# Performance work log

Measured on AMD Instinct MI355X. Metric: run time of the kernel, lower is better.

## Reference

```python
import jax, jax.numpy as jnp
import numpy as np

B, S, E = 32, 128, 128
NQ, NS = 100000, 512
QN, SN = 4, 10
S_MAX = 4
NEG = -1e30


def setup_inputs() -> dict:
    key = jax.random.key(0)
    ks = jax.random.split(key, 24)
    def nrm(k, shape, sc):
        return jax.random.normal(k, shape, jnp.float32) * sc
    inp = {}
    inp['question'] = jax.random.randint(ks[0], (B, S), 0, NQ, jnp.int32)
    inp['response'] = jax.random.randint(ks[1], (B, S), 0, 2, jnp.int32)
    inp['mask'] = jax.random.randint(ks[2], (B, S), 0, 2, jnp.int32)
    inp['q_neighbors'] = jax.random.randint(ks[3], (NQ, QN), 0, NS, jnp.int32)
    inp['s_neighbors'] = jax.random.randint(ks[4], (NS, SN), 0, NQ, jnp.int32)
    sidx = jax.random.randint(ks[5], (NQ, S_MAX), 0, NS, jnp.int32)
    inp['qs_table'] = jnp.zeros((NQ, NS), jnp.float32).at[jnp.arange(NQ)[:, None], sidx].set(1.0)
    inp['emb_q'] = nrm(ks[6], (NQ, E), 1.0)
    inp['emb_s'] = nrm(ks[7], (NS, E), 1.0)
    inp['emb_r'] = nrm(ks[8], (2, E), 1.0)
    s_in = 1.0 / np.sqrt(2 * E).astype(np.float32)
    s_e = 1.0 / np.sqrt(E).astype(np.float32)
    inp['W_ih'] = nrm(ks[9], (4 * E, 2 * E), s_in)
    inp['b_ih'] = nrm(ks[10], (4 * E,), s_in)
    inp['b_hh'] = nrm(ks[11], (4 * E,), s_in)
    inp['W_agg'] = nrm(ks[12], (3, E, E), s_e)
    inp['b_agg'] = nrm(ks[13], (3, E), s_e)
    inp['W_last'] = nrm(ks[14], (E, E), s_e)
    inp['b_last'] = nrm(ks[15], (E,), s_e)
    inp['W_query'] = nrm(ks[16], (E, E), s_e)
    inp['b_query'] = nrm(ks[17], (E,), s_e)
    inp['W_key'] = nrm(ks[18], (E, E), s_e)
    inp['b_key'] = nrm(ks[19], (E,), s_e)
    inp['w_W'] = nrm(ks[20], (2 * E,), s_in)
    inp['b_W'] = nrm(ks[21], (), s_in)
    return inp


def _forward(question, response, mask, q_neighbors, s_neighbors, qs_table,
             emb_q, emb_s, emb_r, W_ih, b_ih, b_hh, W_agg, b_agg, W_last, b_last,
             W_query, b_query, W_key, b_key, w_W, b_W):
    Bq, Sq = question.shape
    Ed = emb_q.shape[1]
    AGG = W_agg.shape[0]
    w_q, w_k = w_W[:Ed], w_W[Ed:]
    c_pad = jnp.tanh(b_query) @ w_k  # attention logit piece of an all-zero padded state
    pos = jnp.arange(Sq)

    def step(state_history, xs):
        t, q_t, r_t, m_t, q_next = xs
        # ---- multi-hop neighbor gather (q -> s -> q -> s) ----
        n1 = q_neighbors[q_t]              # [B,QN] skill ids
        n2 = s_neighbors[n1]               # [B,QN,SN] question ids
        n3 = q_neighbors[n2]               # [B,QN,SN,QN] skill ids
        e = [emb_q[q_t], emb_s[n1], emb_q[n2], emb_s[n3]]
        # triangular mean-aggregate (dropout is identity in eval mode)
        for i in range(AGG):
            for j in range(AGG - i):
                e[j] = jnp.tanh((e[j + 1].mean(-2) + e[j]) @ W_agg[j].T + b_agg[j])
        agg = jnp.tanh(e[0] @ W_last.T + b_last)
        emb_qt = jnp.where((m_t == 1)[:, None], agg, emb_q[q_t])
        # ---- LSTMCell with zero initial (h, c): W_hh @ 0 drops out, b_hh remains ----
        x = jnp.concatenate([emb_qt, emb_r[r_t]], -1)
        gates = x @ W_ih.T + b_ih + b_hh
        gi, gf, gg, go = jnp.split(gates, 4, -1)
        h = jax.nn.sigmoid(go) * jnp.tanh(jax.nn.sigmoid(gi) * jnp.tanh(gg))
        # ---- skills related to next question; zero-padded rows contribute exactly 0 ----
        vals, sidx = jax.lax.top_k(qs_table[q_next], S_MAX)
        emb_sk = emb_s[sidx] * (vals > 0.0)[..., None]
        qs_concat = jnp.concatenate([emb_q[q_next][:, None], emb_sk], 1)  # [B,1+S_MAX,E]
        # ---- hard recap: history steps whose question is a 2-hop neighbor of q_next ----
        q_rel = s_neighbors[q_neighbors[q_next]].reshape(Bq, -1)          # [B,QN*SN]
        matches = (question[:, :, None] == q_rel[:, None, :]).any(-1) & (pos[None, :] < t)
        n_sel = matches.sum(-1)
        P = (jnp.max(n_sel) - n_sel).astype(jnp.float32)  # zero-pad count to per-batch max
        # ---- predict: MLP_W(concat(Q,K)) is rank-1 => logit = a[b,q] + c[b,s] ----
        a = jnp.tanh(qs_concat @ W_key.T + b_key) @ w_q + b_W             # [B,Qd]
        c_hist = jnp.tanh(state_history @ W_query.T + b_query) @ w_k      # [B,S]
        c_cur = jnp.tanh(h @ W_query.T + b_query) @ w_k                   # [B]
        lh = jnp.where(matches[:, None, :], a[:, :, None] + c_hist[:, None, :], NEG)
        lc = a + c_cur[:, None]
        lp = a + c_pad
        m = jnp.maximum(jnp.maximum(lh.max(-1), lc), lp)
        Eh = jnp.exp(lh - m[:, :, None])
        Ec = jnp.exp(lc - m)
        Ep = jnp.exp(lp - m)
        g_hist = jnp.einsum('bqe,bse->bqs', qs_concat, state_history)
        g_cur = jnp.einsum('bqe,be->bq', qs_concat, h)
        denom = Eh.sum(-1) + Ec + P[:, None] * Ep  # zero-pad states counted analytically
        num = (Eh * g_hist).sum(-1) + Ec * g_cur   # pads multiply g=0 -> no numerator term
        y = jax.nn.sigmoid(jnp.sum(num / denom, axis=1))
        # original skips the state write at t == 0 (slot 0 stays zero forever)
        state_history = state_history.at[:, t].set(jnp.where(t > 0, h, jnp.zeros_like(h)))
        return state_history, y

    ts = jnp.arange(Sq - 1)
    xs = (ts, question[:, :-1].T, response[:, :-1].T, mask[:, :-1].T, question[:, 1:].T)
    init = jnp.zeros((Bq, Sq, Ed), jnp.float32)
    _, ys = jax.lax.scan(step, init, xs)
    return jnp.zeros((Bq, Sq), jnp.float32).at[:, 0].set(0.5).at[:, 1:].set(ys.T)


def reference(question, response, mask, q_neighbors, s_neighbors, qs_table,
              emb_q, emb_s, emb_r, W_ih, b_ih, b_hh, W_agg, b_agg, W_last, b_last,
              W_query, b_query, W_key, b_key, w_W, b_W):
    return _forward(question, response, mask, q_neighbors, s_neighbors, qs_table,
                    emb_q, emb_s, emb_r, W_ih, b_ih, b_hh, W_agg, b_agg, W_last, b_last,
                    W_query, b_query, W_key, b_key, w_W, b_W)
```

## Files before the change

### kernel.cpp

```cpp
#include <hip/hip_runtime.h>
#include <stdint.h>

#define NB 32
#define SEQ 128
#define EMB 128
#define NSTEP 127
#define NS 512

__device__ __forceinline__ float ftanh(float x){ float e=__expf(2.f*x); return 1.f-2.f/(e+1.f); }
__device__ __forceinline__ float fsig(float x){ return 1.f/(1.f+__expf(-x)); }
__device__ __forceinline__ float4 ld4(const float* p){ return *(const float4*)p; }

#define FMA4(acc, xv, a0, a1, a2, a3) \
  acc.x = fmaf(xv.x, a0.x, fmaf(xv.y, a1.x, fmaf(xv.z, a2.x, fmaf(xv.w, a3.x, acc.x)))); \
  acc.y = fmaf(xv.x, a0.y, fmaf(xv.y, a1.y, fmaf(xv.z, a2.y, fmaf(xv.w, a3.y, acc.y)))); \
  acc.z = fmaf(xv.x, a0.z, fmaf(xv.y, a1.z, fmaf(xv.z, a2.z, fmaf(xv.w, a3.z, acc.z)))); \
  acc.w = fmaf(xv.x, a0.w, fmaf(xv.y, a1.w, fmaf(xv.z, a2.w, fmaf(xv.w, a3.w, acc.w))));

template<int K, int XS>
__device__ __forceinline__ void gemm8(const float* __restrict__ WT, int NEtot,
                                      const float* Xl, const float* __restrict__ bias,
                                      float* outb)
{
  const int tid = threadIdx.x;
  const int et = tid & 31;
  const int rt = tid >> 5;
  const float* wp = WT + et*4;
  const float* xr = Xl + rt*XS;
  constexpr int G = K/4;
  float4 acc = {0.f,0.f,0.f,0.f};
  float4 w0 = ld4(wp);
  float4 w1 = ld4(wp + NEtot);
  float4 w2 = ld4(wp + 2*NEtot);
  float4 w3 = ld4(wp + 3*NEtot);
  const float* wq = wp + (size_t)4*NEtot;
  float4 m0 = ld4(wq);
  float4 m1 = ld4(wq + NEtot);
  float4 m2 = ld4(wq + 2*NEtot);
  float4 m3 = ld4(wq + 3*NEtot);
  #pragma unroll 2
  for (int g = 0; g + 2 < G; g += 2) {
    const float* wa = wp + (size_t)(4*(g+2))*NEtot;
    float4 n0 = ld4(wa);
    float4 n1 = ld4(wa + NEtot);
    float4 n2 = ld4(wa + 2*NEtot);
    float4 n3 = ld4(wa + 3*NEtot);
    float4 xa = ld4(xr + 4*g);
    FMA4(acc, xa, w0, w1, w2, w3);
    w0=n0; w1=n1; w2=n2; w3=n3;
    const float* wb = wp + (size_t)(4*(g+3))*NEtot;
    float4 o0 = ld4(wb);
    float4 o1 = ld4(wb + NEtot);
    float4 o2 = ld4(wb + 2*NEtot);
    float4 o3 = ld4(wb + 3*NEtot);
    float4 xb = ld4(xr + 4*(g+1));
    FMA4(acc, xb, m0, m1, m2, m3);
    m0=o0; m1=o1; m2=o2; m3=o3;
  }
  {
    float4 xa = ld4(xr + 4*(G-2));
    FMA4(acc, xa, w0, w1, w2, w3);
    float4 xb = ld4(xr + 4*(G-1));
    FMA4(acc, xb, m0, m1, m2, m3);
  }
  float4 bb = ld4(bias + et*4);
  acc.x+=bb.x; acc.y+=bb.y; acc.z+=bb.z; acc.w+=bb.w;
  *(float4*)(outb + rt*132 + et*4) = acc;
}

template<int K, int XS>
__device__ __forceinline__ void gemm16(const float* __restrict__ WT, int NEtot,
                                       const float* Xl, const float* __restrict__ bias,
                                       float* outb)
{
  const int tid = threadIdx.x;
  const int et = tid & 31;
  const int rt = tid >> 5;
  const float* wp = WT + et*4;
  const float* xr = Xl + (size_t)(rt*4)*XS;
  constexpr int G = K/4;
  float4 a0 = {0.f,0.f,0.f,0.f};
  float4 a1 = {0.f,0.f,0.f,0.f};
  float4 a2 = {0.f,0.f,0.f,0.f};
  float4 a3 = {0.f,0.f,0.f,0.f};
  float4 w0 = ld4(wp);
  float4 w1 = ld4(wp + NEtot);
  float4 w2 = ld4(wp + 2*NEtot);
  float4 w3 = ld4(wp + 3*NEtot);
  const float* wq = wp + (size_t)4*NEtot;
  float4 m0 = ld4(wq);
  float4 m1 = ld4(wq + NEtot);
  float4 m2 = ld4(wq + 2*NEtot);
  float4 m3 = ld4(wq + 3*NEtot);
  #pragma unroll 2
  for (int g = 0; g + 2 < G; g += 2) {
    const float* wa = wp + (size_t)(4*(g+2))*NEtot;
    float4 n0 = ld4(wa);
    float4 n1 = ld4(wa + NEtot);
    float4 n2 = ld4(wa + 2*NEtot);
    float4 n3 = ld4(wa + 3*NEtot);
    float4 xa0 = ld4(xr + 4*g);
    float4 xa1 = ld4(xr + XS + 4*g);
    float4 xa2 = ld4(xr + 2*XS + 4*g);
    float4 xa3 = ld4(xr + 3*XS + 4*g);
    FMA4(a0, xa0, w0, w1, w2, w3);
    FMA4(a1, xa1, w0, w1, w2, w3);
    FMA4(a2, xa2, w0, w1, w2, w3);
    FMA4(a3, xa3, w0, w1, w2, w3);
    w0=n0; w1=n1; w2=n2; w3=n3;
    const float* wb = wp + (size_t)(4*(g+3))*NEtot;
    float4 o0 = ld4(wb);
    float4 o1 = ld4(wb + NEtot);
    float4 o2 = ld4(wb + 2*NEtot);
    float4 o3 = ld4(wb + 3*NEtot);
    float4 xb0 = ld4(xr + 4*(g+1));
    float4 xb1 = ld4(xr + XS + 4*(g+1));
    float4 xb2 = ld4(xr + 2*XS + 4*(g+1));
    float4 xb3 = ld4(xr + 3*XS + 4*(g+1));
    FMA4(a0, xb0, m0, m1, m2, m3);
    FMA4(a1, xb1, m0, m1, m2, m3);
    FMA4(a2, xb2, m0, m1, m2, m3);
    FMA4(a3, xb3, m0, m1, m2, m3);
    m0=o0; m1=o1; m2=o2; m3=o3;
  }
  {
    float4 xa0 = ld4(xr + 4*(G-2));
    float4 xa1 = ld4(xr + XS + 4*(G-2));
    float4 xa2 = ld4(xr + 2*XS + 4*(G-2));
    float4 xa3 = ld4(xr + 3*XS + 4*(G-2));
    FMA4(a0, xa0, w0, w1, w2, w3);
    FMA4(a1, xa1, w0, w1, w2, w3);
    FMA4(a2, xa2, w0, w1, w2, w3);
    FMA4(a3, xa3, w0, w1, w2, w3);
    float4 xb0 = ld4(xr + 4*(G-1));
    float4 xb1 = ld4(xr + XS + 4*(G-1));
    float4 xb2 = ld4(xr + 2*XS + 4*(G-1));
    float4 xb3 = ld4(xr + 3*XS + 4*(G-1));
    FMA4(a0, xb0, m0, m1, m2, m3);
    FMA4(a1, xb1, m0, m1, m2, m3);
    FMA4(a2, xb2, m0, m1, m2, m3);
    FMA4(a3, xb3, m0, m1, m2, m3);
  }
  float4 bb = ld4(bias + et*4);
  a0.x+=bb.x; a0.y+=bb.y; a0.z+=bb.z; a0.w+=bb.w;
  a1.x+=bb.x; a1.y+=bb.y; a1.z+=bb.z; a1.w+=bb.w;
  a2.x+=bb.x; a2.y+=bb.y; a2.z+=bb.z; a2.w+=bb.w;
  a3.x+=bb.x; a3.y+=bb.y; a3.z+=bb.z; a3.w+=bb.w;
  float* ob = outb + (size_t)(rt*4)*132 + et*4;
  *(float4*)(ob)         = a0;
  *(float4*)(ob + 132)   = a1;
  *(float4*)(ob + 2*132) = a2;
  *(float4*)(ob + 3*132) = a3;
}

__global__ __launch_bounds__(256) void k_T(
    const float* __restrict__ W_agg, const float* __restrict__ W_last,
    const float* __restrict__ W_query, const float* __restrict__ W_ih,
    const float* __restrict__ b_ih, const float* __restrict__ b_hh,
    const float* __restrict__ b_query, const float* __restrict__ w_W,
    float* __restrict__ WT012, float* __restrict__ WLT, float* __restrict__ WQT,
    float* __restrict__ WIHT, float* __restrict__ BIH, float* __restrict__ CPAD,
    float* __restrict__ G1, int* __restrict__ Pmaxi)
{
  const int gid = blockIdx.x*256 + threadIdx.x;
  const int gsz = gridDim.x*256;
  for (int i = gid; i < 49152; i += gsz) {
    int j = i >> 14, rem = i & 16383, k = rem >> 7, e = rem & 127;
    WT012[i] = W_agg[j*16384 + e*128 + k];
  }
  for (int i = gid; i < 16384; i += gsz) {
    int k = i >> 7, e = i & 127;
    WLT[i] = W_last[e*128 + k];
    WQT[i] = W_query[e*128 + k];
  }
  for (int i = gid; i < 131072; i += gsz) {
    int k = i >> 9, e = i & 511;
    WIHT[i] = W_ih[e*256 + k];
  }
  for (int i = gid; i < 65536; i += gsz) G1[i] = 0.f;
  if (gid < 512) BIH[gid] = b_ih[gid] + b_hh[gid];
  if (gid < 128) Pmaxi[gid] = 0;
  if (blockIdx.x == 0) {
    __shared__ float red[256];
    float v = (threadIdx.x < 128) ? ftanh(b_query[threadIdx.x]) * w_W[128 + threadIdx.x] : 0.f;
    red[threadIdx.x] = v; __syncthreads();
    #pragma unroll
    for (int s = 128; s > 0; s >>= 1) {
      if (threadIdx.x < s) red[threadIdx.x] += red[threadIdx.x + s];
      __syncthreads();
    }
    if (threadIdx.x == 0) CPAD[0] = red[0];
  }
}

__global__ __launch_bounds__(128) void k_pre(
    const int* __restrict__ s_neighbors, const int* __restrict__ q_neighbors,
    const float* __restrict__ emb_q, const float* __restrict__ emb_s,
    const float* __restrict__ WT012, const float* __restrict__ b_agg,
    float* __restrict__ E1, float* __restrict__ G1)
{
  __shared__ float XA[4*132];
  __shared__ float XB[4*132];
  __shared__ int idx[40];
  __shared__ int n3[16];
  const int tid = threadIdx.x;
  const int blk = blockIdx.x;
  if (blk < 128) {
    const int s0 = blk*4;
    if (tid < 40) idx[tid] = s_neighbors[s0*10 + tid];
    __syncthreads();
    {
      int r = tid >> 5, e4 = (tid & 31) << 2;
      float4 a = ld4(emb_s + (size_t)(s0+r)*128 + e4);
      float sx=0,sy=0,sz=0,sw=0;
      #pragma unroll
      for (int jj = 0; jj < 10; ++jj) {
        float4 q = ld4(emb_q + (size_t)idx[r*10+jj]*128 + e4);
        sx+=q.x; sy+=q.y; sz+=q.z; sw+=q.w;
      }
      float4 o; o.x=a.x+0.1f*sx; o.y=a.y+0.1f*sy; o.z=a.z+0.1f*sz; o.w=a.w+0.1f*sw;
      *(float4*)(XA + r*132 + e4) = o;
    }
    __syncthreads();
    gemm8<128,132>(WT012 + 16384, 128, XA, b_agg + 128, XB);
    __syncthreads();
    for (int f = tid; f < 512; f += 128) {
      int r = f >> 7, e = f & 127;
      E1[(size_t)(s0+r)*128 + e] = ftanh(XB[r*132 + e]);
    }
  } else {
    const int p0 = (blk-128)*4;
    if (tid < 4) idx[tid] = s_neighbors[p0 + tid];
    __syncthreads();
    if (tid < 16) n3[tid] = q_neighbors[(size_t)idx[tid>>2]*4 + (tid&3)];
    __syncthreads();
    {
      int r = tid >> 5, e4 = (tid & 31) << 2;
      float4 a = ld4(emb_q + (size_t)idx[r]*128 + e4);
      float sx=0,sy=0,sz=0,sw=0;
      #pragma unroll
      for (int k = 0; k < 4; ++k) {
        float4 q = ld4(emb_s + (size_t)n3[r*4+k]*128 + e4);
        sx+=q.x; sy+=q.y; sz+=q.z; sw+=q.w;
      }
      float4 o; o.x=a.x+0.25f*sx; o.y=a.y+0.25f*sy; o.z=a.z+0.25f*sz; o.w=a.w+0.25f*sw;
      *(float4*)(XA + r*132 + e4) = o;
    }
    __syncthreads();
    gemm8<128,132>(WT012 + 32768, 128, XA, b_agg + 256, XB);
    __syncthreads();
    for (int f = tid; f < 512; f += 128) {
      int r = f >> 7, e = f & 127;
      atomicAdd(&G1[(size_t)((p0+r)/10)*128 + e], ftanh(XB[r*132 + e]));
    }
  }
}

__global__ __launch_bounds__(128) void k_pre2(
    const float* __restrict__ E1, const float* __restrict__ G1,
    const float* __restrict__ WT012, const float* __restrict__ b_agg,
    float* __restrict__ E2)
{
  __shared__ float XA[4*132];
  __shared__ float XB[4*132];
  const int tid = threadIdx.x;
  const int s0 = blockIdx.x*4;
  for (int f = tid; f < 512; f += 128) {
    int r = f >> 7, e = f & 127;
    XA[r*132 + e] = 0.1f*G1[(size_t)(s0+r)*128 + e] + E1[(size_t)(s0+r)*128 + e];
  }
  __syncthreads();
  gemm8<128,132>(WT012 + 16384, 128, XA, b_agg + 128, XB);
  __syncthreads();
  for (int f = tid; f < 512; f += 128) {
    int r = f >> 7, e = f & 127;
    E2[(size_t)(s0+r)*128 + e] = ftanh(XB[r*132 + e]);
  }
}

__global__ __launch_bounds__(128) void k_chain(
    const int* __restrict__ question, const int* __restrict__ response,
    const int* __restrict__ maskp, const int* __restrict__ q_neighbors,
    const float* __restrict__ emb_q, const float* __restrict__ emb_s,
    const float* __restrict__ emb_r,
    const float* __restrict__ WT012, const float* __restrict__ WLT,
    const float* __restrict__ WQT, const float* __restrict__ WIHT,
    const float* __restrict__ BIH,
    const float* __restrict__ b_agg, const float* __restrict__ b_last,
    const float* __restrict__ b_query, const float* __restrict__ w_W,
    const float* __restrict__ E1, const float* __restrict__ E2,
    float* __restrict__ Hfull, float* __restrict__ Cq)
{
  __shared__ float XA[16*132];
  __shared__ float XB[16*132];
  __shared__ float M1[16*132];
  __shared__ float M2[16*132];
  __shared__ float XC[16*264];
  __shared__ int qts[16], rts[16], mts[16], n1s[64];

  const int tid = threadIdx.x;
  const int blk = blockIdx.x;

  if (tid < 16) {
    int rid = blk*16 + tid;
    int b = rid / 127, t = rid - b*127;
    qts[tid] = question[b*SEQ + t];
    rts[tid] = response[b*SEQ + t];
    mts[tid] = maskp[b*SEQ + t];
  }
  __syncthreads();
  if (tid < 64) n1s[tid] = q_neighbors[(size_t)qts[tid>>2]*4 + (tid&3)];
  __syncthreads();
  {
    const int e4 = (tid & 31) << 2;
    for (int rr = tid >> 5; rr < 16; rr += 4) {
      const int* nn = n1s + rr*4;
      float4 a = ld4(emb_q + (size_t)qts[rr]*128 + e4);
      float s1x=0,s1y=0,s1z=0,s1w=0, s2x=0,s2y=0,s2z=0,s2w=0, s3x=0,s3y=0,s3z=0,s3w=0;
      #pragma unroll
      for (int i = 0; i < 4; ++i) {
        float4 q1 = ld4(emb_s + (size_t)nn[i]*128 + e4);
        float4 q2 = ld4(E1 + (size_t)nn[i]*128 + e4);
        float4 q3 = ld4(E2 + (size_t)nn[i]*128 + e4);
        s1x+=q1.x; s1y+=q1.y; s1z+=q1.z; s1w+=q1.w;
        s2x+=q2.x; s2y+=q2.y; s2z+=q2.z; s2w+=q2.w;
        s3x+=q3.x; s3y+=q3.y; s3z+=q3.z; s3w+=q3.w;
      }
      float4 o; o.x=a.x+0.25f*s1x; o.y=a.y+0.25f*s1y; o.z=a.z+0.25f*s1z; o.w=a.w+0.25f*s1w;
      *(float4*)(XA + rr*132 + e4) = o;
      float4 p; p.x=0.25f*s2x; p.y=0.25f*s2y; p.z=0.25f*s2z; p.w=0.25f*s2w;
      *(float4*)(M1 + rr*132 + e4) = p;
      float4 u; u.x=0.25f*s3x; u.y=0.25f*s3y; u.z=0.25f*s3z; u.w=0.25f*s3w;
      *(float4*)(M2 + rr*132 + e4) = u;
    }
  }
  __syncthreads();
  gemm16<128,132>(WT012, 128, XA, b_agg, XB);
  __syncthreads();
  for (int f = tid; f < 2112; f += 128) XB[f] = M1[f] + ftanh(XB[f]);
  __syncthreads();
  gemm16<128,132>(WT012, 128, XB, b_agg, XA);
  __syncthreads();
  for (int f = tid; f < 2112; f += 128) XA[f] = M2[f] + ftanh(XA[f]);
  __syncthreads();
  gemm16<128,132>(WT012, 128, XA, b_agg, XB);
  __syncthreads();
  for (int f = tid; f < 2112; f += 128) XB[f] = ftanh(XB[f]);
  __syncthreads();
  gemm16<128,132>(WLT, 128, XB, b_last, XA);
  __syncthreads();
  for (int f = tid; f < 2048; f += 128) {
    int r = f >> 7, e = f & 127;
    float agg = ftanh(XA[r*132 + e]);
    XC[r*264 + e] = (mts[r] == 1) ? agg : emb_q[(size_t)qts[r]*128 + e];
    XC[r*264 + 128 + e] = emb_r[rts[r]*128 + e];
  }
  __syncthreads();
  gemm16<256,264>(WIHT,       512, XC, BIH,       XA);
  gemm16<256,264>(WIHT + 256, 512, XC, BIH + 256, XB);
  gemm16<256,264>(WIHT + 384, 512, XC, BIH + 384, M1);
  __syncthreads();
  for (int f = tid; f < 2048; f += 128) {
    int r = f >> 7, e = f & 127;
    float gi = XA[r*132 + e], gg = XB[r*132 + e], go = M1[r*132 + e];
    float h = fsig(go) * ftanh(fsig(gi) * ftanh(gg));
    XC[r*264 + e] = h;
    Hfull[(size_t)(blk*16 + r)*128 + e] = h;
  }
  __syncthreads();
  gemm16<128,264>(WQT, 128, XC, b_query, XA);
  __syncthreads();
  {
    const int et = tid & 31, rt = tid >> 5;
    float4 wv = ld4(w_W + 128 + et*4);
    for (int rr = rt; rr < 16; rr += 4) {
      float4 o = ld4(XA + rr*132 + et*4);
      float s = ftanh(o.x)*wv.x + ftanh(o.y)*wv.y + ftanh(o.z)*wv.z + ftanh(o.w)*wv.w;
      #pragma unroll
      for (int off = 16; off > 0; off >>= 1) s += __shfl_down(s, off);
      if (et == 0) Cq[blk*16 + rr] = s;
    }
  }
}

__global__ __launch_bounds__(64) void k_match(
    const int* __restrict__ question, const int* __restrict__ q_neighbors,
    const int* __restrict__ s_neighbors,
    int* __restrict__ nsel, unsigned long long* __restrict__ mwords,
    int* __restrict__ Pmaxi)
{
  __shared__ int qr[40];
  const int tid = threadIdx.x;
  const int t = blockIdx.x;
  const int b = blockIdx.y;
  const int q_next = question[b*SEQ + t + 1];
  if (tid < 40)
    qr[tid] = s_neighbors[(size_t)q_neighbors[(size_t)q_next*4 + tid/10]*10 + tid%10];
  __syncthreads();
  int q0 = question[b*SEQ + tid];
  int q1 = question[b*SEQ + 64 + tid];
  bool p0 = false, p1 = false;
  #pragma unroll 8
  for (int i = 0; i < 40; ++i) { p0 |= (q0 == qr[i]); p1 |= (q1 == qr[i]); }
  p0 &= (tid < t);
  p1 &= (64 + tid < t);
  unsigned long long w0 = __ballot(p0);
  unsigned long long w1 = __ballot(p1);
  if (tid == 0) {
    mwords[((size_t)b*NSTEP + t)*2 + 0] = w0;
    mwords[((size_t)b*NSTEP + t)*2 + 1] = w1;
    int ns = __popcll(w0) + __popcll(w1);
    nsel[b*NSTEP + t] = ns;
    atomicMax(&Pmaxi[t], ns);
  }
}

__device__ __forceinline__ float wredsum(float v) {
  #pragma unroll
  for (int o = 32; o > 0; o >>= 1) v += __shfl_down(v, o);
  return v;
}
__device__ __forceinline__ float wredmax(float v) {
  #pragma unroll
  for (int o = 32; o > 0; o >>= 1) v = fmaxf(v, __shfl_down(v, o));
  return v;
}

__global__ __launch_bounds__(128) void k_attn(
    const int* __restrict__ question, const float* __restrict__ qs_table,
    const float* __restrict__ emb_q, const float* __restrict__ emb_s,
    const float* __restrict__ CPAD,
    const float* __restrict__ Hfull, const float* __restrict__ Cq,
    const int* __restrict__ nsel, const unsigned long long* __restrict__ mwords,
    const int* __restrict__ Pmaxi, float* __restrict__ out)
{
  __shared__ float us[128];
  __shared__ int cols[8];
  __shared__ int cnt;
  __shared__ float smx[2];
  __shared__ float s3[2][3];
  const int tid = threadIdx.x;
  const int wid = tid >> 6;
  const int bid = blockIdx.x;
  const int b = bid / NSTEP, t = bid % NSTEP;
  const size_t bt = (size_t)b*NSTEP + t;
  const int q_next = question[b*SEQ + t + 1];

  if (tid == 0) cnt = 0;
  __syncthreads();
  {
    float4 v = ld4(qs_table + (size_t)q_next*NS + tid*4);
    if (v.x > 0.f) { int p = atomicAdd(&cnt, 1); if (p < 8) cols[p] = tid*4; }
    if (v.y > 0.f) { int p = atomicAdd(&cnt, 1); if (p < 8) cols[p] = tid*4+1; }
    if (v.z > 0.f) { int p = atomicAdd(&cnt, 1); if (p < 8) cols[p] = tid*4+2; }
    if (v.w > 0.f) { int p = atomicAdd(&cnt, 1); if (p < 8) cols[p] = tid*4+3; }
  }
  __syncthreads();
  const int nc = min(cnt, 4);
  {
    float ue = emb_q[(size_t)q_next*EMB + tid];
    for (int i = 0; i < nc; ++i) ue += emb_s[(size_t)cols[i]*EMB + tid];
    us[tid] = ue;
  }
  const float c_pad = CPAD[0];
  const float P = (float)(Pmaxi[t] - nsel[bt]);

  const unsigned long long w0 = mwords[bt*2 + 0];
  const unsigned long long w1 = mwords[bt*2 + 1];
  const bool matched = (tid < 64) ? ((w0 >> tid) & 1ull)
                                  : ((w1 >> (tid - 64)) & 1ull);
  const float c_cur = Cq[bt];
  float Cp = matched ? ((tid == 0) ? c_pad : Cq[(size_t)b*NSTEP + tid]) : -3.0e38f;
  float mh = wredmax(Cp);
  if ((tid & 63) == 0) smx[wid] = mh;
  __syncthreads();
  float M = fmaxf(fmaxf(smx[0], smx[1]), fmaxf(c_cur, c_pad));
  float wgt = matched ? __expf(Cp - M) : 0.f;
  float dotp = 0.f;
  if (matched && tid >= 1) {
    const float* hp = Hfull + ((size_t)b*NSTEP + tid)*EMB;
    float s = 0.f;
    #pragma unroll 8
    for (int e = 0; e < 128; e += 4) {
      float4 h4 = ld4(hp + e);
      s = fmaf(us[e],h4.x, fmaf(us[e+1],h4.y, fmaf(us[e+2],h4.z, fmaf(us[e+3],h4.w, s))));
    }
    dotp = s;
  }
  float gcp = us[tid] * Hfull[bt*EMB + tid];
  float a0 = wredsum(wgt);
  float a1 = wredsum(wgt * dotp);
  float a2 = wredsum(gcp);
  if ((tid & 63) == 0) { s3[wid][0] = a0; s3[wid][1] = a1; s3[wid][2] = a2; }
  __syncthreads();
  if (tid == 0) {
    float Sexp = s3[0][0] + s3[1][0];
    float Snum = s3[0][1] + s3[1][1];
    float gc   = s3[0][2] + s3[1][2];
    float Ec = __expf(c_cur - M), Ep = __expf(c_pad - M);
    float D = Sexp + Ec + P * Ep;
    float numt = Snum + Ec * gc;
    out[b*SEQ + t + 1] = fsig(numt / D);
    if (t == 0) out[b*SEQ] = 0.5f;
  }
}

extern "C" void kernel_launch(void* const* d_in, const int* in_sizes, int n_in,
                              void* d_out, int out_size, void* d_ws, size_t ws_size,
                              hipStream_t stream) {
  const int* question    = (const int*)d_in[0];
  const int* response    = (const int*)d_in[1];
  const int* maskp       = (const int*)d_in[2];
  const int* q_neighbors = (const int*)d_in[3];
  const int* s_neighbors = (const int*)d_in[4];
  const float* qs_table  = (const float*)d_in[5];
  const float* emb_q     = (const float*)d_in[6];
  const float* emb_s     = (const float*)d_in[7];
  const float* emb_r     = (const float*)d_in[8];
  const float* W_ih      = (const float*)d_in[9];
  const float* b_ih      = (const float*)d_in[10];
  const float* b_hh      = (const float*)d_in[11];
  const float* W_agg     = (const float*)d_in[12];
  const float* b_agg     = (const float*)d_in[13];
  const float* W_last    = (const float*)d_in[14];
  const float* b_last    = (const float*)d_in[15];
  const float* W_query   = (const float*)d_in[16];
  const float* b_query   = (const float*)d_in[17];
  const float* w_W       = (const float*)d_in[20];
  float* out = (float*)d_out;

  float* ws = (float*)d_ws;
  float* WT012 = ws;
  float* WLT   = ws + 49152;
  float* WQT   = ws + 65536;
  float* WIHT  = ws + 81920;
  float* BIH   = ws + 212992;
  float* CPAD  = ws + 213504;
  float* E1    = ws + 213520;
  float* G1    = ws + 279056;
  float* E2    = ws + 344592;
  float* Hfull = ws + 410128;
  float* Cq    = ws + 930320;
  int*   Pmaxi = (int*)(ws + 934384);
  int*   nselp = (int*)(ws + 934512);
  unsigned long long* mwords =
      (unsigned long long*)(((uintptr_t)(ws + 938576) + 15) & ~(uintptr_t)15);

  k_T<<<dim3(512), dim3(256), 0, stream>>>(
      W_agg, W_last, W_query, W_ih, b_ih, b_hh, b_query, w_W,
      WT012, WLT, WQT, WIHT, BIH, CPAD, G1, Pmaxi);
  k_pre<<<dim3(1408), dim3(128), 0, stream>>>(
      s_neighbors, q_neighbors, emb_q, emb_s, WT012, b_agg, E1, G1);
  k_pre2<<<dim3(128), dim3(128), 0, stream>>>(E1, G1, WT012, b_agg, E2);
  k_chain<<<dim3(254), dim3(128), 0, stream>>>(
      question, response, maskp, q_neighbors, emb_q, emb_s, emb_r,
      WT012, WLT, WQT, WIHT, BIH, b_agg, b_last, b_query, w_W,
      E1, E2, Hfull, Cq);
  k_match<<<dim3(NSTEP, NB), dim3(64), 0, stream>>>(
      question, q_neighbors, s_neighbors, nselp, mwords, Pmaxi);
  k_attn<<<dim3(NB*NSTEP), dim3(128), 0, stream>>>(
      question, qs_table, emb_q, emb_s, CPAD, Hfull, Cq,
      nselp, mwords, Pmaxi, out);
}
```

Before: 422.5 us.

## Fold neighbor-match kernel into chain kernel and double chain block size

```diff
diff --git a/kernel.cpp b/kernel.cpp
--- a/kernel.cpp
+++ b/kernel.cpp
@@ -69,20 +69,18 @@
 }
 
 template<int K, int XS>
-__device__ __forceinline__ void gemm16(const float* __restrict__ WT, int NEtot,
-                                       const float* Xl, const float* __restrict__ bias,
-                                       float* outb)
+__device__ __forceinline__ void gemm2(const float* __restrict__ WT, int NEtot,
+                                      const float* Xl, const float* __restrict__ bias,
+                                      float* outb)
 {
   const int tid = threadIdx.x;
   const int et = tid & 31;
   const int rt = tid >> 5;
   const float* wp = WT + et*4;
-  const float* xr = Xl + (size_t)(rt*4)*XS;
+  const float* xr = Xl + (size_t)(rt*2)*XS;
   constexpr int G = K/4;
   float4 a0 = {0.f,0.f,0.f,0.f};
   float4 a1 = {0.f,0.f,0.f,0.f};
-  float4 a2 = {0.f,0.f,0.f,0.f};
-  float4 a3 = {0.f,0.f,0.f,0.f};
   float4 w0 = ld4(wp);
   float4 w1 = ld4(wp + NEtot);
   float4 w2 = ld4(wp + 2*NEtot);
@@ -101,12 +99,8 @@
     float4 n3 = ld4(wa + 3*NEtot);
     float4 xa0 = ld4(xr + 4*g);
     float4 xa1 = ld4(xr + XS + 4*g);
-    float4 xa2 = ld4(xr + 2*XS + 4*g);
-    float4 xa3 = ld4(xr + 3*XS + 4*g);
     FMA4(a0, xa0, w0, w1, w2, w3);
     FMA4(a1, xa1, w0, w1, w2, w3);
-    FMA4(a2, xa2, w0, w1, w2, w3);
-    FMA4(a3, xa3, w0, w1, w2, w3);
     w0=n0; w1=n1; w2=n2; w3=n3;
     const float* wb = wp + (size_t)(4*(g+3))*NEtot;
     float4 o0 = ld4(wb);
@@ -115,42 +109,26 @@
     float4 o3 = ld4(wb + 3*NEtot);
     float4 xb0 = ld4(xr + 4*(g+1));
     float4 xb1 = ld4(xr + XS + 4*(g+1));
-    float4 xb2 = ld4(xr + 2*XS + 4*(g+1));
-    float4 xb3 = ld4(xr + 3*XS + 4*(g+1));
     FMA4(a0, xb0, m0, m1, m2, m3);
     FMA4(a1, xb1, m0, m1, m2, m3);
-    FMA4(a2, xb2, m0, m1, m2, m3);
-    FMA4(a3, xb3, m0, m1, m2, m3);
     m0=o0; m1=o1; m2=o2; m3=o3;
   }
   {
     float4 xa0 = ld4(xr + 4*(G-2));
     float4 xa1 = ld4(xr + XS + 4*(G-2));
-    float4 xa2 = ld4(xr + 2*XS + 4*(G-2));
-    float4 xa3 = ld4(xr + 3*XS + 4*(G-2));
     FMA4(a0, xa0, w0, w1, w2, w3);
     FMA4(a1, xa1, w0, w1, w2, w3);
-    FMA4(a2, xa2, w0, w1, w2, w3);
-    FMA4(a3, xa3, w0, w1, w2, w3);
     float4 xb0 = ld4(xr + 4*(G-1));
     float4 xb1 = ld4(xr + XS + 4*(G-1));
-    float4 xb2 = ld4(xr + 2*XS + 4*(G-1));
-    float4 xb3 = ld4(xr + 3*XS + 4*(G-1));
     FMA4(a0, xb0, m0, m1, m2, m3);
     FMA4(a1, xb1, m0, m1, m2, m3);
-    FMA4(a2, xb2, m0, m1, m2, m3);
-    FMA4(a3, xb3, m0, m1, m2, m3);
   }
   float4 bb = ld4(bias + et*4);
   a0.x+=bb.x; a0.y+=bb.y; a0.z+=bb.z; a0.w+=bb.w;
   a1.x+=bb.x; a1.y+=bb.y; a1.z+=bb.z; a1.w+=bb.w;
-  a2.x+=bb.x; a2.y+=bb.y; a2.z+=bb.z; a2.w+=bb.w;
-  a3.x+=bb.x; a3.y+=bb.y; a3.z+=bb.z; a3.w+=bb.w;
-  float* ob = outb + (size_t)(rt*4)*132 + et*4;
-  *(float4*)(ob)         = a0;
-  *(float4*)(ob + 132)   = a1;
-  *(float4*)(ob + 2*132) = a2;
-  *(float4*)(ob + 3*132) = a3;
+  float* ob = outb + (size_t)(rt*2)*132 + et*4;
+  *(float4*)(ob)       = a0;
+  *(float4*)(ob + 132) = a1;
 }
 
 __global__ __launch_bounds__(256) void k_T(
@@ -278,9 +256,10 @@
   }
 }
 
-__global__ __launch_bounds__(128) void k_chain(
+__global__ __launch_bounds__(256) void k_chain(
     const int* __restrict__ question, const int* __restrict__ response,
     const int* __restrict__ maskp, const int* __restrict__ q_neighbors,
+    const int* __restrict__ s_neighbors,
     const float* __restrict__ emb_q, const float* __restrict__ emb_s,
     const float* __restrict__ emb_r,
     const float* __restrict__ WT012, const float* __restrict__ WLT,
@@ -289,7 +268,9 @@
     const float* __restrict__ b_agg, const float* __restrict__ b_last,
     const float* __restrict__ b_query, const float* __restrict__ w_W,
     const float* __restrict__ E1, const float* __restrict__ E2,
-    float* __restrict__ Hfull, float* __restrict__ Cq)
+    float* __restrict__ Hfull, float* __restrict__ Cq,
+    int* __restrict__ nsel, unsigned long long* __restrict__ mwords,
+    int* __restrict__ Pmaxi)
 {
   __shared__ float XA[16*132];
   __shared__ float XB[16*132];
@@ -313,7 +294,7 @@
   __syncthreads();
   {
     const int e4 = (tid & 31) << 2;
-    for (int rr = tid >> 5; rr < 16; rr += 4) {
+    for (int rr = tid >> 5; rr < 16; rr += 8) {
       const int* nn = n1s + rr*4;
       float4 a = ld4(emb_q + (size_t)qts[rr]*128 + e4);
       float s1x=0,s1y=0,s1z=0,s1w=0, s2x=0,s2y=0,s2z=0,s2w=0, s3x=0,s3y=0,s3z=0,s3w=0;
@@ -335,32 +316,32 @@
     }
   }
   __syncthreads();
-  gemm16<128,132>(WT012, 128, XA, b_agg, XB);
-  __syncthreads();
-  for (int f = tid; f < 2112; f += 128) XB[f] = M1[f] + ftanh(XB[f]);
-  __syncthreads();
-  gemm16<128,132>(WT012, 128, XB, b_agg, XA);
-  __syncthreads();
-  for (int f = tid; f < 2112; f += 128) XA[f] = M2[f] + ftanh(XA[f]);
-  __syncthreads();
-  gemm16<128,132>(WT012, 128, XA, b_agg, XB);
-  __syncthreads();
-  for (int f = tid; f < 2112; f += 128) XB[f] = ftanh(XB[f]);
-  __syncthreads();
-  gemm16<128,132>(WLT, 128, XB, b_last, XA);
-  __syncthreads();
-  for (int f = tid; f < 2048; f += 128) {
+  gemm2<128,132>(WT012, 128, XA, b_agg, XB);
+  __syncthreads();
+  for (int f = tid; f < 2112; f += 256) XB[f] = M1[f] + ftanh(XB[f]);
+  __syncthreads();
+  gemm2<128,132>(WT012, 128, XB, b_agg, XA);
+  __syncthreads();
+  for (int f = tid; f < 2112; f += 256) XA[f] = M2[f] + ftanh(XA[f]);
+  __syncthreads();
+  gemm2<128,132>(WT012, 128, XA, b_agg, XB);
+  __syncthreads();
+  for (int f = tid; f < 2112; f += 256) XB[f] = ftanh(XB[f]);
+  __syncthreads();
+  gemm2<128,132>(WLT, 128, XB, b_last, XA);
+  __syncthreads();
+  for (int f = tid; f < 2048; f += 256) {
     int r = f >> 7, e = f & 127;
     float agg = ftanh(XA[r*132 + e]);
     XC[r*264 + e] = (mts[r] == 1) ? agg : emb_q[(size_t)qts[r]*128 + e];
     XC[r*264 + 128 + e] = emb_r[rts[r]*128 + e];
   }
   __syncthreads();
-  gemm16<256,264>(WIHT,       512, XC, BIH,       XA);
-  gemm16<256,264>(WIHT + 256, 512, XC, BIH + 256, XB);
-  gemm16<256,264>(WIHT + 384, 512, XC, BIH + 384, M1);
-  __syncthreads();
-  for (int f = tid; f < 2048; f += 128) {
+  gemm2<256,264>(WIHT,       512, XC, BIH,       XA);
+  gemm2<256,264>(WIHT + 256, 512, XC, BIH + 256, XB);
+  gemm2<256,264>(WIHT + 384, 512, XC, BIH + 384, M1);
+  __syncthreads();
+  for (int f = tid; f < 2048; f += 256) {
     int r = f >> 7, e = f & 127;
     float gi = XA[r*132 + e], gg = XB[r*132 + e], go = M1[r*132 + e];
     float h = fsig(go) * ftanh(fsig(gi) * ftanh(gg));
@@ -368,12 +349,12 @@
     Hfull[(size_t)(blk*16 + r)*128 + e] = h;
   }
   __syncthreads();
-  gemm16<128,264>(WQT, 128, XC, b_query, XA);
+  gemm2<128,264>(WQT, 128, XC, b_query, XA);
   __syncthreads();
   {
     const int et = tid & 31, rt = tid >> 5;
     float4 wv = ld4(w_W + 128 + et*4);
-    for (int rr = rt; rr < 16; rr += 4) {
+    for (int rr = rt; rr < 16; rr += 8) {
       float4 o = ld4(XA + rr*132 + et*4);
       float s = ftanh(o.x)*wv.x + ftanh(o.y)*wv.y + ftanh(o.z)*wv.z + ftanh(o.w)*wv.w;
       #pragma unroll
@@ -381,37 +362,37 @@
       if (et == 0) Cq[blk*16 + rr] = s;
     }
   }
-}
-
-__global__ __launch_bounds__(64) void k_match(
-    const int* __restrict__ question, const int* __restrict__ q_neighbors,
-    const int* __restrict__ s_neighbors,
-    int* __restrict__ nsel, unsigned long long* __restrict__ mwords,
-    int* __restrict__ Pmaxi)
-{
-  __shared__ int qr[40];
-  const int tid = threadIdx.x;
-  const int t = blockIdx.x;
-  const int b = blockIdx.y;
-  const int q_next = question[b*SEQ + t + 1];
-  if (tid < 40)
-    qr[tid] = s_neighbors[(size_t)q_neighbors[(size_t)q_next*4 + tid/10]*10 + tid%10];
-  __syncthreads();
-  int q0 = question[b*SEQ + tid];
-  int q1 = question[b*SEQ + 64 + tid];
-  bool p0 = false, p1 = false;
-  #pragma unroll 8
-  for (int i = 0; i < 40; ++i) { p0 |= (q0 == qr[i]); p1 |= (q1 == qr[i]); }
-  p0 &= (tid < t);
-  p1 &= (64 + tid < t);
-  unsigned long long w0 = __ballot(p0);
-  unsigned long long w1 = __ballot(p1);
-  if (tid == 0) {
-    mwords[((size_t)b*NSTEP + t)*2 + 0] = w0;
-    mwords[((size_t)b*NSTEP + t)*2 + 1] = w1;
-    int ns = __popcll(w0) + __popcll(w1);
-    nsel[b*NSTEP + t] = ns;
-    atomicMax(&Pmaxi[t], ns);
+  {
+    const int wv = tid >> 6;
+    const int ln = tid & 63;
+    for (int rr = wv; rr < 16; rr += 4) {
+      int rid = blk*16 + rr;
+      int b = rid / 127, t = rid - b*127;
+      int q_next = question[b*SEQ + t + 1];
+      int qrv = 0;
+      if (ln < 40)
+        qrv = s_neighbors[(size_t)q_neighbors[(size_t)q_next*4 + ln/10]*10 + ln%10];
+      int q0 = question[b*SEQ + ln];
+      int q1 = question[b*SEQ + 64 + ln];
+      bool p0 = false, p1 = false;
+      #pragma unroll 8
+      for (int i = 0; i < 40; ++i) {
+        int qv = __shfl(qrv, i);
+        p0 |= (q0 == qv); p1 |= (q1 == qv);
+      }
+      p0 &= (ln < t);
+      p1 &= (64 + ln < t);
+      unsigned long long w0 = __ballot(p0);
+      unsigned long long w1 = __ballot(p1);
+      if (ln == 0) {
+        size_t bt = (size_t)b*NSTEP + t;
+        mwords[bt*2 + 0] = w0;
+        mwords[bt*2 + 1] = w1;
+        int ns = __popcll(w0) + __popcll(w1);
+        nsel[bt] = ns;
+        atomicMax(&Pmaxi[t], ns);
+      }
+    }
   }
 }
 
@@ -552,12 +533,10 @@
   k_pre<<<dim3(1408), dim3(128), 0, stream>>>(
       s_neighbors, q_neighbors, emb_q, emb_s, WT012, b_agg, E1, G1);
   k_pre2<<<dim3(128), dim3(128), 0, stream>>>(E1, G1, WT012, b_agg, E2);
-  k_chain<<<dim3(254), dim3(128), 0, stream>>>(
-      question, response, maskp, q_neighbors, emb_q, emb_s, emb_r,
+  k_chain<<<dim3(254), dim3(256), 0, stream>>>(
+      question, response, maskp, q_neighbors, s_neighbors, emb_q, emb_s, emb_r,
       WT012, WLT, WQT, WIHT, BIH, b_agg, b_last, b_query, w_W,
-      E1, E2, Hfull, Cq);
-  k_match<<<dim3(NSTEP, NB), dim3(64), 0, stream>>>(
-      question, q_neighbors, s_neighbors, nselp, mwords, Pmaxi);
+      E1, E2, Hfull, Cq, nselp, mwords, Pmaxi);
   k_attn<<<dim3(NB*NSTEP), dim3(128), 0, stream>>>(
       question, qs_table, emb_q, emb_s, CPAD, Hfull, Cq,
       nselp, mwords, Pmaxi, out);
```

After: 399.1 us. 5.5% less time.
